# Performance work log

Hardware: AMD Instinct MI355X
Metric: run time of the kernel (lower is better)

The kernel has to match this reference:

```python
import jax, jax.numpy as jnp
from jax import lax
import numpy as np

BN_EPS = 1e-3


def _bn_train(x, gamma, beta):
    # training-mode BatchNorm2d: batch stats over (N, H, W), biased variance
    mean = jnp.mean(x, axis=(0, 2, 3), keepdims=True)
    var = jnp.var(x, axis=(0, 2, 3), keepdims=True)
    g = gamma[None, :, None, None]
    b = beta[None, :, None, None]
    return (x - mean) * lax.rsqrt(var + BN_EPS) * g + b


def _pointwise(x, w, b, gamma, beta):
    # 1x1 conv + BN + relu (reluM = clamp(min=0))
    y = jnp.einsum('bchw,oc->bohw', x, w) + b[None, :, None, None]
    return jnp.maximum(_bn_train(y, gamma, beta), 0.0)


def _depthwise1d(x, w, b, gamma, beta):
    # depthwise (1,5) conv, zero pad width by 2 each side, BN, clamp(-8,8)
    C = w.shape[0]
    k = w[:, None, None, :]  # [C,1,1,5]
    y = lax.conv_general_dilated(
        x, k, window_strides=(1, 1), padding=[(0, 0), (2, 2)],
        feature_group_count=C,
        dimension_numbers=('NCHW', 'OIHW', 'NCHW'))
    y = y + b[None, :, None, None]
    return jnp.clip(_bn_train(y, gamma, beta), -8.0, 8.0)


def _iir(x, w3, gamma, beta):
    # y[0] = (a+b+c)*x[0];  y[r] = a*x[r] + b*x[r-1] + c*y[r-1]
    a = w3[0][:, None]  # w_curr_inp, [C,1]
    b = w3[1][:, None]  # w_prev_inp
    c = w3[2][:, None]  # w_prev_out
    xT = jnp.moveaxis(x, 2, 0)  # [H,B,C,W]
    y0 = (a + b + c) * xT[0]

    def step(y_prev, xs):
        x_curr, x_prev = xs
        y = a * x_curr + b * x_prev + c * y_prev
        return y, y

    _, ys = lax.scan(step, y0, (xT[1:], xT[:-1]))
    y = jnp.concatenate([y0[None], ys], axis=0)
    y = jnp.moveaxis(y, 0, 2)  # back to [B,C,H,W]
    return jnp.clip(_bn_train(y, gamma, beta), -8.0, 8.0)


def _process_unit(x, u, iir_w, iir_gamma, iir_beta, dw_w, dw_b, dw_gamma,
                  dw_beta, pw_w, pw_b, pw_gamma, pw_beta):
    h = _iir(x, iir_w[u], iir_gamma[u], iir_beta[u])
    h = _depthwise1d(h, dw_w[u], dw_b[u], dw_gamma[u], dw_beta[u])
    return _pointwise(h, pw_w[u], pw_b[u], pw_gamma[u], pw_beta[u])


def setup_inputs() -> dict:
    key = jax.random.key(0)
    ks = jax.random.split(key, 16)
    B, Cin, Cout, H, W = 4, 36, 72, 256, 256
    return {
        'x': jax.random.normal(ks[0], (B, Cin, H, W), jnp.float32),
        'expand_w': jax.random.normal(ks[1], (Cout, Cin), jnp.float32),
        'expand_b': jax.random.normal(ks[2], (Cout,), jnp.float32),
        'expand_gamma': jax.random.uniform(ks[3], (Cout,), jnp.float32),
        'expand_beta': jax.random.normal(ks[4], (Cout,), jnp.float32),
        'iir_w': jax.random.uniform(ks[5], (4, 3, Cout), jnp.float32),
        'iir_gamma': jax.random.uniform(ks[6], (4, Cout), jnp.float32),
        'iir_beta': jax.random.normal(ks[7], (4, Cout), jnp.float32),
        'dw_w': jax.random.normal(ks[8], (4, Cout, 5), jnp.float32),
        'dw_b': jax.random.normal(ks[9], (4, Cout), jnp.float32),
        'dw_gamma': jax.random.uniform(ks[10], (4, Cout), jnp.float32),
        'dw_beta': jax.random.normal(ks[11], (4, Cout), jnp.float32),
        'pw_w': jax.random.normal(ks[12], (4, Cout, Cout), jnp.float32),
        'pw_b': jax.random.normal(ks[13], (4, Cout), jnp.float32),
        'pw_gamma': jax.random.uniform(ks[14], (4, Cout), jnp.float32),
        'pw_beta': jax.random.normal(ks[15], (4, Cout), jnp.float32),
    }


def reference(x, expand_w, expand_b, expand_gamma, expand_beta, iir_w,
              iir_gamma, iir_beta, dw_w, dw_b, dw_gamma, dw_beta, pw_w,
              pw_b, pw_gamma, pw_beta):
    h = _pointwise(x, expand_w, expand_b, expand_gamma, expand_beta)
    unit = lambda z, u: _process_unit(z, u, iir_w, iir_gamma, iir_beta, dw_w,
                                      dw_b, dw_gamma, dw_beta, pw_w, pw_b,
                                      pw_gamma, pw_beta)
    h = h + unit(unit(h, 0), 1)
    h = h + unit(unit(h, 2), 3)
    return h
```

## Files before the change

### kernel.cpp

```cpp
#include <hip/hip_runtime.h>
#include <hip/hip_fp16.h>

#define BBATCH 4
#define CCH 72
#define HROW 256
#define WCOL 256
#define HWSZ (HROW*WCOL)
#define NPC (BBATCH*HROW*WCOL)
#define BNEPS 1e-3f
#define NSH 64
#define SST 144

typedef unsigned short u16;
typedef unsigned int u32;
typedef _Float16 h8 __attribute__((ext_vector_type(8)));
typedef float f32x4 __attribute__((ext_vector_type(4)));

__device__ __forceinline__ float h2f(u16 h_){ return __half2float(__ushort_as_half(h_)); }
__device__ __forceinline__ u16 f2h(float f){ return __half_as_ushort(__float2half(f)); }
__device__ __forceinline__ u32 pack2(float a, float b){ return (u32)f2h(a) | ((u32)f2h(b)<<16); }
__device__ __forceinline__ float clip8(float v){ return fminf(fmaxf(v,-8.f),8.f); }

__device__ __forceinline__ void get_ss_wave(int c, int lane, const float* __restrict__ pstat,
                                            const float* __restrict__ gam, const float* __restrict__ bet,
                                            float& sc, float& sh){
  float s = pstat[lane*SST + c];
  float q = pstat[lane*SST + 72 + c];
  #pragma unroll
  for (int off=32; off; off>>=1){ s += __shfl_xor(s,off); q += __shfl_xor(q,off); }
  float mean = s * (1.0f/(float)NPC);
  float var  = q * (1.0f/(float)NPC) - mean*mean;
  sc = gam[c] * rsqrtf(var + BNEPS);
  sh = bet[c] - mean*sc;
}

__global__ __launch_bounds__(256) void k_prep(const float* __restrict__ ew,
    const float* __restrict__ pwall, u16* __restrict__ Wp)
{
  for (int e = blockIdx.x*256 + threadIdx.x; e < 14*3200; e += gridDim.x*256){
    int slab = e / 3200, rem = e - slab*3200;
    int row = rem / 40, col = rem - row*40;
    float w = 0.f;
    if (slab < 2){
      int c = slab*32 + col;
      if (row < 72 && col < 32 && c < 36) w = ew[row*36 + c];
    } else {
      int u = (slab-2)/3, kb = (slab-2)%3;
      int c = kb*32 + col;
      if (row < 72 && col < 32) w = pwall[u*5184 + row*72 + c];
    }
    Wp[e] = f2h(w);
  }
}

template<int CIN, int RAW>
__global__ __launch_bounds__(512) void k_pw(const void* __restrict__ in_,
    u16* __restrict__ out, const u16* __restrict__ Wp,
    const float* __restrict__ pstat,
    const float* __restrict__ pgam, const float* __restrict__ pbet,
    float* __restrict__ ostat)
{
  constexpr int KB   = (CIN + 31) / 32;
  constexpr int CPAD = KB * 32;
  constexpr int CST  = CPAD + 1;
  constexpr int XST  = 18;
  constexpr int XSZ  = 16 * CST * XST;
  constexpr int ESZ  = 72 * 264;
  constexpr int SSZ  = (XSZ > ESZ) ? XSZ : ESZ;
  constexpr int NXT  = (CIN*32 + 511) / 512;

  __shared__ u16 xs[SSZ];
  __shared__ float tsc[80], tsh[80];
  __shared__ float pp4[4][72], pq4[4][72];
  __shared__ float sst[72], sqt[72];

  const int tid  = threadIdx.x;
  const int lane = tid & 63;
  const int wid  = tid >> 6;
  const int g    = lane >> 4;
  const int li   = lane & 15;
  const int b    = blockIdx.x >> 8;
  const int hrow = blockIdx.x & 255;

  uint4  xr[NXT];
  float4 xa[NXT], xb[NXT];
  #pragma unroll
  for (int it = 0; it < NXT; ++it){
    int e = tid + it*512;
    if (e < CIN*32){
      int c = e >> 5, o8 = e & 31;
      if constexpr (RAW){
        const float* ip = (const float*)in_ + (size_t)b*CIN*HWSZ + (size_t)c*HWSZ + (size_t)hrow*WCOL + o8*8;
        xa[it] = *(const float4*)ip;
        xb[it] = *(const float4*)(ip+4);
      } else {
        const u16* ip = (const u16*)in_ + (size_t)b*CIN*HWSZ + (size_t)c*HWSZ + (size_t)hrow*WCOL + o8*8;
        xr[it] = *(const uint4*)ip;
      }
    }
  }

  if (tid < 72){ sst[tid] = 0.f; sqt[tid] = 0.f; }

  for (int e = tid; e < (CPAD-CIN)*32; e += 512){
    int c = CIN + (e >> 5), o8 = e & 31;
    int pxt = o8 >> 1, pp = (o8 & 1) * 8;
    *(uint4*)&xs[(pxt*CST + c)*XST + pp] = make_uint4(0,0,0,0);
  }

  if constexpr (!RAW){
    int sg = tid >> 7, c = tid & 127;
    if (c < 72){
      float s = 0.f, q = 0.f;
      #pragma unroll
      for (int k2 = 0; k2 < 16; ++k2){
        s += pstat[(sg*16 + k2)*SST + c];
        q += pstat[(sg*16 + k2)*SST + 72 + c];
      }
      pp4[sg][c] = s; pq4[sg][c] = q;
    }
    __syncthreads();
    if (tid < CIN){
      float s = pp4[0][tid] + pp4[1][tid] + pp4[2][tid] + pp4[3][tid];
      float q = pq4[0][tid] + pq4[1][tid] + pq4[2][tid] + pq4[3][tid];
      float mean = s * (1.0f/(float)NPC);
      float var  = q * (1.0f/(float)NPC) - mean*mean;
      float scv  = pgam[tid] * rsqrtf(var + BNEPS);
      tsc[tid] = scv;
      tsh[tid] = pbet[tid] - mean*scv;
    }
  }
  __syncthreads();

  #pragma unroll
  for (int it = 0; it < NXT; ++it){
    int e = tid + it*512;
    if (e < CIN*32){
      int c = e >> 5, o8 = e & 31;
      int pxt = o8 >> 1, pp = (o8 & 1) * 8;
      float v[8];
      if constexpr (RAW){
        v[0]=xa[it].x; v[1]=xa[it].y; v[2]=xa[it].z; v[3]=xa[it].w;
        v[4]=xb[it].x; v[5]=xb[it].y; v[6]=xb[it].z; v[7]=xb[it].w;
      } else {
        u32 rr[4] = {xr[it].x, xr[it].y, xr[it].z, xr[it].w};
        float scv = tsc[c], shv = tsh[c];
        #pragma unroll
        for (int q2=0; q2<4; ++q2){
          v[2*q2]   = clip8(h2f((u16)rr[q2])*scv + shv);
          v[2*q2+1] = clip8(h2f((u16)(rr[q2]>>16))*scv + shv);
        }
      }
      uint4 pk;
      pk.x = pack2(v[0],v[1]); pk.y = pack2(v[2],v[3]);
      pk.z = pack2(v[4],v[5]); pk.w = pack2(v[6],v[7]);
      *(uint4*)&xs[(pxt*CST + c)*XST + pp] = pk;
    }
  }
  __syncthreads();

  f32x4 acc[5][2];
  #pragma unroll
  for (int mt=0; mt<5; ++mt){ acc[mt][0] = (f32x4){0,0,0,0}; acc[mt][1] = (f32x4){0,0,0,0}; }
  const int pxA = wid*2, pxB = wid*2 + 1;
  #pragma unroll
  for (int kb = 0; kb < KB; ++kb){
    h8 bf0, bf1;
    #pragma unroll
    for (int j = 0; j < 8; ++j){
      bf0[j] = *(const _Float16*)&xs[(pxA*CST + kb*32 + g*8 + j)*XST + li];
      bf1[j] = *(const _Float16*)&xs[(pxB*CST + kb*32 + g*8 + j)*XST + li];
    }
    #pragma unroll
    for (int mt = 0; mt < 5; ++mt){
      h8 ah = *(const h8*)(Wp + (size_t)(kb*80 + mt*16 + li)*40 + g*8);
      acc[mt][0] = __builtin_amdgcn_mfma_f32_16x16x32_f16(ah, bf0, acc[mt][0], 0, 0, 0);
      acc[mt][1] = __builtin_amdgcn_mfma_f32_16x16x32_f16(ah, bf1, acc[mt][1], 0, 0, 0);
    }
  }
  __syncthreads();

  #pragma unroll
  for (int mt = 0; mt < 5; ++mt){
    int o = mt*16 + g*4;
    if (o < 72){
      #pragma unroll
      for (int t2 = 0; t2 < 2; ++t2){
        int px = (wid*2 + t2)*16 + li;
        #pragma unroll
        for (int r = 0; r < 4; ++r)
          xs[(o + r)*264 + px] = f2h(acc[mt][t2][r]);
      }
    }
  }
  __syncthreads();

  #pragma unroll
  for (int it = 0; it < 5; ++it){
    int e = tid + it*512;
    if (e < 72*32){
      int o = e >> 5, m = e & 31;
      uint4 v = *(const uint4*)&xs[o*264 + m*8];
      u32 rr[4] = {v.x, v.y, v.z, v.w};
      float s = 0.f, q = 0.f;
      #pragma unroll
      for (int q2=0; q2<4; ++q2){
        float a  = h2f((u16)rr[q2]);
        float bq = h2f((u16)(rr[q2]>>16));
        s += a + bq;
        q = fmaf(a,a,q); q = fmaf(bq,bq,q);
      }
      *(uint4*)(out + (size_t)b*CCH*HWSZ + (size_t)o*HWSZ + (size_t)hrow*WCOL + m*8) = v;
      #pragma unroll
      for (int off = 1; off <= 16; off <<= 1){ s += __shfl_xor(s, off); q += __shfl_xor(q, off); }
      if ((lane & 31) == 0){ atomicAdd(&sst[o], s); atomicAdd(&sqt[o], q); }
    }
  }
  __syncthreads();
  if (tid < 72){
    float* oshard = ostat + (size_t)(blockIdx.x & (NSH-1))*SST;
    atomicAdd(oshard + tid,      sst[tid]);
    atomicAdd(oshard + 72 + tid, sqt[tid]);
  }
}

template<int MODE>
__global__ __launch_bounds__(256) void k_iir(const u16* __restrict__ in, u16* __restrict__ out,
    const float* __restrict__ wabc, u16* __restrict__ hbuf,
    const float* __restrict__ pstat,
    const float* __restrict__ pgam, const float* __restrict__ pbet,
    float* __restrict__ ostat)
{
  const int tid = threadIdx.x;
  const int bc = blockIdx.x;
  const int c = bc % CCH;
  float sc, sh; get_ss_wave(c, tid&63, pstat, pgam, pbet, sc, sh);
  const float ka = wabc[c], kb = wabc[CCH+c], kcc = wabc[2*CCH+c];
  const size_t base = (size_t)bc*HWSZ + tid;
  float xprev=0.f, yprev=0.f, lsum=0.f, lssq=0.f;

  float a0[16], a1[16], r0[16], r1[16];

  auto LOADC = [&](int hb, float* xv, float* rv){
    #pragma unroll
    for (int j=0;j<16;++j){
      size_t idx = base + (size_t)(hb+j)*WCOL;
      xv[j] = h2f(in[idx]);
      if (MODE==2) rv[j] = h2f(hbuf[idx]);
    }
  };
  auto COMPC = [&](int hb, const float* xv, const float* rv){
    float x[16];
    #pragma unroll
    for (int j=0;j<16;++j){
      float v = fmaxf(xv[j]*sc + sh, 0.f);
      if (MODE==1) hbuf[base + (size_t)(hb+j)*WCOL] = f2h(v);
      if (MODE==2){ v += rv[j]; hbuf[base + (size_t)(hb+j)*WCOL] = f2h(v); }
      x[j] = v;
    }
    if (hb == 0){ xprev = x[0]; yprev = x[0]; }
    float t[16];
    t[0] = fmaf(ka, x[0], kb*xprev);
    #pragma unroll
    for (int j=1;j<16;++j) t[j] = fmaf(ka, x[j], kb*x[j-1]);
    #pragma unroll
    for (int j=0;j<16;++j){
      yprev = fmaf(kcc, yprev, t[j]);
      out[base + (size_t)(hb+j)*WCOL] = f2h(yprev);
      lsum += yprev; lssq = fmaf(yprev,yprev,lssq);
    }
    xprev = x[15];
  };

  LOADC(0, a0, r0);
  #pragma unroll
  for (int hb = 0; hb < HROW; hb += 32){
    LOADC(hb+16, a1, r1);
    COMPC(hb, a0, r0);
    if (hb+32 < HROW) LOADC(hb+32, a0, r0);
    COMPC(hb+16, a1, r1);
  }

  #pragma unroll
  for (int off=32; off; off>>=1){ lsum += __shfl_xor(lsum,off); lssq += __shfl_xor(lssq,off); }
  __shared__ float rs[4], rq[4];
  if ((tid&63)==0){ rs[tid>>6]=lsum; rq[tid>>6]=lssq; }
  __syncthreads();
  if (tid==0){
    float* oshard = ostat + (size_t)(blockIdx.x & (NSH-1))*SST;
    atomicAdd(oshard + c,      rs[0]+rs[1]+rs[2]+rs[3]);
    atomicAdd(oshard + 72 + c, rq[0]+rq[1]+rq[2]+rq[3]);
  }
}

__global__ __launch_bounds__(256) void k_dw(const u16* __restrict__ in, u16* __restrict__ out,
    const float* __restrict__ wgt,
    const float* __restrict__ pstat,
    const float* __restrict__ pgam, const float* __restrict__ pbet,
    float* __restrict__ ostat)
{
  __shared__ float xs[8*264];
  __shared__ float rs[4], rq[4];
  const int tid = threadIdx.x;
  const int ht = blockIdx.x & 31;
  const int bc = blockIdx.x >> 5;
  const int c = bc % CCH;
  float sc, sh; get_ss_wave(c, tid&63, pstat, pgam, pbet, sc, sh);
  const float w0=wgt[c*5+0], w1=wgt[c*5+1], w2=wgt[c*5+2], w3=wgt[c*5+3], w4=wgt[c*5+4];
  const size_t base = (size_t)bc*HWSZ + (size_t)ht*(8*WCOL);

  if (tid < 64){
    int r = tid>>3, k = tid&7;
    xs[r*264 + (k<4 ? k : 256+k)] = 0.f;
  }
  const int r = tid >> 5, m = tid & 31;
  {
    uint4 v = *(const uint4*)(in + base + (size_t)r*WCOL + m*8);
    u32 rr[4] = {v.x, v.y, v.z, v.w};
    float f[8];
    #pragma unroll
    for (int q=0;q<4;++q){
      f[2*q]   = clip8(h2f((u16)rr[q])*sc + sh);
      f[2*q+1] = clip8(h2f((u16)(rr[q]>>16))*sc + sh);
    }
    float4* dst = (float4*)&xs[r*264 + 4 + m*8];
    dst[0] = make_float4(f[0],f[1],f[2],f[3]);
    dst[1] = make_float4(f[4],f[5],f[6],f[7]);
  }
  __syncthreads();
  float lsum=0.f, lssq=0.f;
  {
    const float* row = &xs[r*264 + m*8];
    float4 a0 = *(const float4*)(row+0);
    float4 a1 = *(const float4*)(row+4);
    float4 a2 = *(const float4*)(row+8);
    float4 a3 = *(const float4*)(row+12);
    float v[16] = {a0.x,a0.y,a0.z,a0.w, a1.x,a1.y,a1.z,a1.w,
                   a2.x,a2.y,a2.z,a2.w, a3.x,a3.y,a3.z,a3.w};
    float o[8];
    #pragma unroll
    for (int j=0;j<8;++j){
      float y = w0*v[j+2];
      y = fmaf(w1, v[j+3], y);
      y = fmaf(w2, v[j+4], y);
      y = fmaf(w3, v[j+5], y);
      y = fmaf(w4, v[j+6], y);
      o[j] = y;
      lsum += y; lssq = fmaf(y,y,lssq);
    }
    *(uint4*)(out + base + (size_t)r*WCOL + m*8) =
        make_uint4(pack2(o[0],o[1]), pack2(o[2],o[3]), pack2(o[4],o[5]), pack2(o[6],o[7]));
  }
  #pragma unroll
  for (int off=32; off; off>>=1){ lsum += __shfl_xor(lsum,off); lssq += __shfl_xor(lssq,off); }
  if ((tid&63)==0){ rs[tid>>6]=lsum; rq[tid>>6]=lssq; }
  __syncthreads();
  if (tid==0){
    float* oshard = ostat + (size_t)(blockIdx.x & (NSH-1))*SST;
    atomicAdd(oshard + c,      rs[0]+rs[1]+rs[2]+rs[3]);
    atomicAdd(oshard + 72 + c, rq[0]+rq[1]+rq[2]+rq[3]);
  }
}

__global__ __launch_bounds__(256) void k_final(const u16* __restrict__ y12, const u16* __restrict__ h1,
    float* __restrict__ outp,
    const float* __restrict__ pstat,
    const float* __restrict__ pgam, const float* __restrict__ pbet)
{
  __shared__ float tsc[CCH], tsh[CCH];
  if (threadIdx.x < CCH){
    int cc = threadIdx.x;
    float s=0.f, q=0.f;
    for (int sh2=0; sh2<NSH; ++sh2){ s += pstat[sh2*SST + cc]; q += pstat[sh2*SST + 72 + cc]; }
    float mean = s * (1.0f/(float)NPC);
    float var  = q * (1.0f/(float)NPC) - mean*mean;
    float scv = pgam[cc] * rsqrtf(var + BNEPS);
    tsc[cc] = scv;
    tsh[cc] = pbet[cc] - mean*scv;
  }
  __syncthreads();
  const size_t TOTALQ = (size_t)BBATCH*CCH*HWSZ/4;
  for (size_t q = (size_t)blockIdx.x*blockDim.x + threadIdx.x; q < TOTALQ;
       q += (size_t)gridDim.x*blockDim.x){
    int cch = (int)((q >> 14) % CCH);
    float sc = tsc[cch], sh = tsh[cch];
    uint2 a = *(const uint2*)(y12 + q*4);
    uint2 b = *(const uint2*)(h1 + q*4);
    float4 o;
    o.x = fmaxf(h2f((u16)a.x)*sc+sh, 0.f)       + h2f((u16)b.x);
    o.y = fmaxf(h2f((u16)(a.x>>16))*sc+sh, 0.f) + h2f((u16)(b.x>>16));
    o.z = fmaxf(h2f((u16)a.y)*sc+sh, 0.f)       + h2f((u16)b.y);
    o.w = fmaxf(h2f((u16)(a.y>>16))*sc+sh, 0.f) + h2f((u16)(b.y>>16));
    *(float4*)(outp + q*4) = o;
  }
}

extern "C" void kernel_launch(void* const* d_in, const int* in_sizes, int n_in,
                              void* d_out, int out_size, void* d_ws, size_t ws_size,
                              hipStream_t stream)
{
  (void)in_sizes; (void)n_in; (void)out_size;
  const float* x   = (const float*)d_in[0];
  const float* ew  = (const float*)d_in[1];
  const float* eg  = (const float*)d_in[3];
  const float* ebt = (const float*)d_in[4];
  const float* iw  = (const float*)d_in[5];
  const float* ig  = (const float*)d_in[6];
  const float* ibt = (const float*)d_in[7];
  const float* dwt = (const float*)d_in[8];
  const float* dg  = (const float*)d_in[10];
  const float* dbt = (const float*)d_in[11];
  const float* pw  = (const float*)d_in[12];
  const float* pg  = (const float*)d_in[14];
  const float* pbt = (const float*)d_in[15];
  float* outp = (float*)d_out;

  const size_t BUFE = (size_t)BBATCH*CCH*HWSZ;
  const size_t BUFB = BUFE*2;
  const size_t STATSB = (size_t)13*NSH*SST*sizeof(float);
  const size_t WPB = (size_t)14*3200*sizeof(u16);
  char* ws = (char*)d_ws;
  u16* A = (u16*)ws;
  u16* H = (u16*)(ws + BUFB);
  u16* B;
  float* stats;
  if (ws_size >= 3*BUFB + STATSB + WPB + 256){
    B = (u16*)(ws + 2*BUFB);
    stats = (float*)(ws + 3*BUFB);
  } else {
    B = (u16*)d_out;
    stats = (float*)(ws + 2*BUFB);
  }
  u16* Wp = (u16*)((char*)stats + STATSB);
  #define ST(s) (stats + (size_t)(s)*NSH*SST)
  #define WSLAB(u) (Wp + (size_t)(2 + 3*(u))*3200)

  hipMemsetAsync(stats, 0, STATSB, stream);

  dim3 blk(256);
  dim3 blkpw(512);
  k_prep<<<18, blk, 0, stream>>>(ew, pw, Wp);
  k_pw<36,1><<<BBATCH*HROW, blkpw, 0, stream>>>((const void*)x, A, Wp,
      nullptr, nullptr, nullptr, ST(0));
  k_iir<1><<<BBATCH*CCH, blk, 0, stream>>>(A, B, iw+0,   H, ST(0), eg, ebt, ST(1));
  k_dw    <<<BBATCH*CCH*32, blk, 0, stream>>>(B, A, dwt+0,    ST(1), ig+0,   ibt+0,   ST(2));
  k_pw<72,0><<<BBATCH*HROW, blkpw, 0, stream>>>(A, B, WSLAB(0), ST(2), dg+0,   dbt+0,   ST(3));
  k_iir<0><<<BBATCH*CCH, blk, 0, stream>>>(B, A, iw+216, nullptr, ST(3), pg+0,  pbt+0,  ST(4));
  k_dw    <<<BBATCH*CCH*32, blk, 0, stream>>>(A, B, dwt+360,  ST(4), ig+72,  ibt+72,  ST(5));
  k_pw<72,0><<<BBATCH*HROW, blkpw, 0, stream>>>(B, A, WSLAB(1), ST(5), dg+72,  dbt+72,  ST(6));
  k_iir<2><<<BBATCH*CCH, blk, 0, stream>>>(A, B, iw+432, H, ST(6), pg+72, pbt+72, ST(7));
  k_dw    <<<BBATCH*CCH*32, blk, 0, stream>>>(B, A, dwt+720,  ST(7), ig+144, ibt+144, ST(8));
  k_pw<72,0><<<BBATCH*HROW, blkpw, 0, stream>>>(A, B, WSLAB(2), ST(8), dg+144, dbt+144, ST(9));
  k_iir<0><<<BBATCH*CCH, blk, 0, stream>>>(B, A, iw+648, nullptr, ST(9), pg+144, pbt+144, ST(10));
  k_dw    <<<BBATCH*CCH*32, blk, 0, stream>>>(A, B, dwt+1080, ST(10), ig+216, ibt+216, ST(11));
  k_pw<72,0><<<BBATCH*HROW, blkpw, 0, stream>>>(B, A, WSLAB(3), ST(11), dg+216, dbt+216, ST(12));
  k_final<<<2048, blk, 0, stream>>>(A, H, outp, ST(12), pg+216, pbt+216);
  #undef ST
  #undef WSLAB
}
```

Baseline: 339.2 us.

## Load pointwise-conv B fragments directly from global memory, skipping LDS staging

The pointwise conv kernel now builds each MFMA B operand by reading activation values straight from global memory per lane, applying the BN scale/shift and clip inline, instead of first loading vectorized rows into registers, converting them, and staging them through a transposed shared-memory tile. This removes one LDS write/read pass and a barrier, and the stats scratch now reuses the shared output buffer. In exchange, global loads become scalar 2- or 4-byte accesses (16 consecutive pixels per lane group) rather than 16-byte vector loads, and padded channels issue redundant reads of channel 0, which may hurt memory efficiency.

```diff
diff --git a/kernel.cpp b/kernel.cpp
--- a/kernel.cpp
+++ b/kernel.cpp
@@ -60,19 +60,12 @@
     const float* __restrict__ pgam, const float* __restrict__ pbet,
     float* __restrict__ ostat)
 {
-  constexpr int KB   = (CIN + 31) / 32;
-  constexpr int CPAD = KB * 32;
-  constexpr int CST  = CPAD + 1;
-  constexpr int XST  = 18;
-  constexpr int XSZ  = 16 * CST * XST;
-  constexpr int ESZ  = 72 * 264;
-  constexpr int SSZ  = (XSZ > ESZ) ? XSZ : ESZ;
-  constexpr int NXT  = (CIN*32 + 511) / 512;
-
-  __shared__ u16 xs[SSZ];
+  constexpr int KB = (CIN + 31) / 32;
+  __shared__ __align__(16) u16 xs[72*264];
   __shared__ float tsc[80], tsh[80];
-  __shared__ float pp4[4][72], pq4[4][72];
   __shared__ float sst[72], sqt[72];
+  float* pp4 = (float*)xs;
+  float* pq4 = pp4 + 320;
 
   const int tid  = threadIdx.x;
   const int lane = tid & 63;
@@ -82,31 +75,7 @@
   const int b    = blockIdx.x >> 8;
   const int hrow = blockIdx.x & 255;
 
-  uint4  xr[NXT];
-  float4 xa[NXT], xb[NXT];
-  #pragma unroll
-  for (int it = 0; it < NXT; ++it){
-    int e = tid + it*512;
-    if (e < CIN*32){
-      int c = e >> 5, o8 = e & 31;
-      if constexpr (RAW){
-        const float* ip = (const float*)in_ + (size_t)b*CIN*HWSZ + (size_t)c*HWSZ + (size_t)hrow*WCOL + o8*8;
-        xa[it] = *(const float4*)ip;
-        xb[it] = *(const float4*)(ip+4);
-      } else {
-        const u16* ip = (const u16*)in_ + (size_t)b*CIN*HWSZ + (size_t)c*HWSZ + (size_t)hrow*WCOL + o8*8;
-        xr[it] = *(const uint4*)ip;
-      }
-    }
-  }
-
   if (tid < 72){ sst[tid] = 0.f; sqt[tid] = 0.f; }
-
-  for (int e = tid; e < (CPAD-CIN)*32; e += 512){
-    int c = CIN + (e >> 5), o8 = e & 31;
-    int pxt = o8 >> 1, pp = (o8 & 1) * 8;
-    *(uint4*)&xs[(pxt*CST + c)*XST + pp] = make_uint4(0,0,0,0);
-  }
 
   if constexpr (!RAW){
     int sg = tid >> 7, c = tid & 127;
@@ -117,68 +86,55 @@
         s += pstat[(sg*16 + k2)*SST + c];
         q += pstat[(sg*16 + k2)*SST + 72 + c];
       }
-      pp4[sg][c] = s; pq4[sg][c] = q;
+      pp4[sg*80 + c] = s; pq4[sg*80 + c] = q;
     }
     __syncthreads();
     if (tid < CIN){
-      float s = pp4[0][tid] + pp4[1][tid] + pp4[2][tid] + pp4[3][tid];
-      float q = pq4[0][tid] + pq4[1][tid] + pq4[2][tid] + pq4[3][tid];
+      float s = pp4[tid] + pp4[80+tid] + pp4[160+tid] + pp4[240+tid];
+      float q = pq4[tid] + pq4[80+tid] + pq4[160+tid] + pq4[240+tid];
       float mean = s * (1.0f/(float)NPC);
       float var  = q * (1.0f/(float)NPC) - mean*mean;
       float scv  = pgam[tid] * rsqrtf(var + BNEPS);
       tsc[tid] = scv;
       tsh[tid] = pbet[tid] - mean*scv;
     }
-  }
-  __syncthreads();
-
-  #pragma unroll
-  for (int it = 0; it < NXT; ++it){
-    int e = tid + it*512;
-    if (e < CIN*32){
-      int c = e >> 5, o8 = e & 31;
-      int pxt = o8 >> 1, pp = (o8 & 1) * 8;
-      float v[8];
+    __syncthreads();
+  }
+
+  const size_t base_in = (size_t)b*CIN*HWSZ + (size_t)hrow*WCOL;
+  const int px0 = wid*32 + li;
+  f32x4 acc[5][2];
+  #pragma unroll
+  for (int mt=0; mt<5; ++mt){ acc[mt][0] = (f32x4){0,0,0,0}; acc[mt][1] = (f32x4){0,0,0,0}; }
+
+  #pragma unroll
+  for (int kb2 = 0; kb2 < KB; ++kb2){
+    h8 bf0, bf1;
+    #pragma unroll
+    for (int j = 0; j < 8; ++j){
+      int c  = kb2*32 + g*8 + j;
+      int cc = (c < CIN) ? c : 0;
+      float v0, v1;
       if constexpr (RAW){
-        v[0]=xa[it].x; v[1]=xa[it].y; v[2]=xa[it].z; v[3]=xa[it].w;
-        v[4]=xb[it].x; v[5]=xb[it].y; v[6]=xb[it].z; v[7]=xb[it].w;
+        const float* ip = (const float*)in_ + base_in + (size_t)cc*HWSZ;
+        v0 = ip[px0]; v1 = ip[px0 + 16];
       } else {
-        u32 rr[4] = {xr[it].x, xr[it].y, xr[it].z, xr[it].w};
-        float scv = tsc[c], shv = tsh[c];
-        #pragma unroll
-        for (int q2=0; q2<4; ++q2){
-          v[2*q2]   = clip8(h2f((u16)rr[q2])*scv + shv);
-          v[2*q2+1] = clip8(h2f((u16)(rr[q2]>>16))*scv + shv);
-        }
+        const u16* ip = (const u16*)in_ + base_in + (size_t)cc*HWSZ;
+        float scv = tsc[cc], shv = tsh[cc];
+        v0 = clip8(h2f(ip[px0])*scv + shv);
+        v1 = clip8(h2f(ip[px0 + 16])*scv + shv);
       }
-      uint4 pk;
-      pk.x = pack2(v[0],v[1]); pk.y = pack2(v[2],v[3]);
-      pk.z = pack2(v[4],v[5]); pk.w = pack2(v[6],v[7]);
-      *(uint4*)&xs[(pxt*CST + c)*XST + pp] = pk;
-    }
-  }
-  __syncthreads();
-
-  f32x4 acc[5][2];
-  #pragma unroll
-  for (int mt=0; mt<5; ++mt){ acc[mt][0] = (f32x4){0,0,0,0}; acc[mt][1] = (f32x4){0,0,0,0}; }
-  const int pxA = wid*2, pxB = wid*2 + 1;
-  #pragma unroll
-  for (int kb = 0; kb < KB; ++kb){
-    h8 bf0, bf1;
-    #pragma unroll
-    for (int j = 0; j < 8; ++j){
-      bf0[j] = *(const _Float16*)&xs[(pxA*CST + kb*32 + g*8 + j)*XST + li];
-      bf1[j] = *(const _Float16*)&xs[(pxB*CST + kb*32 + g*8 + j)*XST + li];
+      bool ok = (c < CIN);
+      bf0[j] = (_Float16)(ok ? v0 : 0.f);
+      bf1[j] = (_Float16)(ok ? v1 : 0.f);
     }
     #pragma unroll
     for (int mt = 0; mt < 5; ++mt){
-      h8 ah = *(const h8*)(Wp + (size_t)(kb*80 + mt*16 + li)*40 + g*8);
+      h8 ah = *(const h8*)(Wp + (size_t)(kb2*80 + mt*16 + li)*40 + g*8);
       acc[mt][0] = __builtin_amdgcn_mfma_f32_16x16x32_f16(ah, bf0, acc[mt][0], 0, 0, 0);
       acc[mt][1] = __builtin_amdgcn_mfma_f32_16x16x32_f16(ah, bf1, acc[mt][1], 0, 0, 0);
     }
   }
-  __syncthreads();
 
   #pragma unroll
   for (int mt = 0; mt < 5; ++mt){
@@ -186,7 +142,7 @@
     if (o < 72){
       #pragma unroll
       for (int t2 = 0; t2 < 2; ++t2){
-        int px = (wid*2 + t2)*16 + li;
+        int px = wid*32 + t2*16 + li;
         #pragma unroll
         for (int r = 0; r < 4; ++r)
           xs[(o + r)*264 + px] = f2h(acc[mt][t2][r]);
```

New measurement: 334.2 us. About the same (-1.5%).
